# Optimization experiments

Measured on AMD Instinct MI355X. Metric: run time of the kernel, lower is better.

The kernel has to match this reference:

```python
import jax, jax.numpy as jnp
import numpy as np

B, S, H, HD, DM = 8, 1024, 16, 64, 1024

def rotate_half(x):
    x1, x2 = x[..., : x.shape[-1] // 2], x[..., x.shape[-1] // 2 :]
    return jnp.concatenate((-x2, x1), axis=-1)

def apply_rope(x, cos, sin):
    return x * cos + rotate_half(x) * sin

def setup_inputs() -> dict:
    key = jax.random.key(0)
    ks = jax.random.split(key, 6)
    T = B * S
    hidden_states = jax.random.normal(ks[0], (T, DM), dtype=jnp.float32)
    scale = 1.0 / np.sqrt(DM)
    q_w = jax.random.normal(ks[1], (DM, DM), dtype=jnp.float32) * scale
    k_w = jax.random.normal(ks[2], (DM, DM), dtype=jnp.float32) * scale
    v_w = jax.random.normal(ks[3], (DM, DM), dtype=jnp.float32) * scale
    o_w = jax.random.normal(ks[4], (DM, DM), dtype=jnp.float32) * scale
    # RoPE tables: positions restart at each segment boundary
    pos = jnp.tile(jnp.arange(S, dtype=jnp.float32), B)           # [T]
    inv_freq = 1.0 / (10000.0 ** (jnp.arange(0, HD, 2, dtype=jnp.float32) / HD))
    ang = pos[:, None] * inv_freq[None, :]                        # [T, HD/2]
    emb = jnp.concatenate([ang, ang], axis=-1)                    # [T, HD]
    cos = jnp.cos(emb)[:, None, :]                                # [T, 1, HD]
    sin = jnp.sin(emb)[:, None, :]
    cu_seqlens = (jnp.arange(B + 1) * S).astype(jnp.int32)        # [B+1]
    return {
        "hidden_states": hidden_states,
        "q_w": q_w, "k_w": k_w, "v_w": v_w, "o_w": o_w,
        "cos": cos, "sin": sin,
        "cu_seqlens": cu_seqlens, "max_seqlen": S,
    }

def reference(hidden_states, q_w, k_w, v_w, o_w, cos, sin, cu_seqlens, max_seqlen):
    T, D = hidden_states.shape
    hd = cos.shape[-1]
    nh = D // hd
    nb = cu_seqlens.shape[0] - 1
    S_ = max_seqlen
    # QKV projections (torch Linear: y = x @ W^T)
    q = (hidden_states @ q_w.T).reshape(T, nh, hd)
    k = (hidden_states @ k_w.T).reshape(T, nh, hd)
    v = (hidden_states @ v_w.T).reshape(T, nh, hd)
    q = apply_rope(q, cos, sin)
    k = apply_rope(k, cos, sin)
    # Equal-length varlen segments -> dense batched causal attention
    q = q.reshape(nb, S_, nh, hd)
    k = k.reshape(nb, S_, nh, hd)
    v = v.reshape(nb, S_, nh, hd)
    scale = 1.0 / np.sqrt(hd).astype(np.float32)
    scores = jnp.einsum("bqhd,bkhd->bhqk", q, k) * scale          # [B,H,S,S]
    causal = jnp.tril(jnp.ones((S_, S_), dtype=bool))
    scores = jnp.where(causal[None, None], scores, jnp.finfo(scores.dtype).min)
    probs = jax.nn.softmax(scores, axis=-1)
    attn = jnp.einsum("bhqk,bkhd->bqhd", probs, v).reshape(T, D)
    return attn @ o_w.T
```

## Files before the change

kernel.cpp:

```cpp
#include <hip/hip_runtime.h>

typedef __attribute__((ext_vector_type(8))) short short8;
typedef __attribute__((ext_vector_type(4))) short short4v;
typedef __attribute__((ext_vector_type(4))) float f32x4;

#define MFMA(a, b, c) __builtin_amdgcn_mfma_f32_16x16x32_bf16((a), (b), (c), 0, 0, 0)
#define GLD16(g, l)                                                            \
  __builtin_amdgcn_global_load_lds(                                            \
      (const __attribute__((address_space(1))) void*)(g),                      \
      (__attribute__((address_space(3))) void*)(l), 16, 0, 0)

static __device__ __forceinline__ float b2f(unsigned short b) {
  union { unsigned u; float f; } u; u.u = ((unsigned)b) << 16; return u.f;
}
static __device__ __forceinline__ unsigned short f2b(float f) {
  union { float f; unsigned u; } u; u.f = f;
  unsigned r = u.u + 0x7FFFu + ((u.u >> 16) & 1u);
  return (unsigned short)(r >> 16);
}
static __device__ __forceinline__ unsigned cvt_pk_bf16(float a, float b) {
  unsigned r;
  asm("v_cvt_pk_bf16_f32 %0, %1, %2" : "=v"(r) : "v"(a), "v"(b));
  return r;
}

__global__ __launch_bounds__(256) void convert_kernel(
    const float* __restrict__ hidden,
    const float* __restrict__ qw, const float* __restrict__ kw,
    const float* __restrict__ vw, const float* __restrict__ ow,
    unsigned short* __restrict__ dst) {
  const int HID4 = 2097152, W4 = 262144, TOT = HID4 + 4 * W4;
  for (int i = blockIdx.x * 256 + threadIdx.x; i < TOT; i += gridDim.x * 256) {
    const float* src; int off;
    if (i < HID4) { src = hidden; off = i; }
    else {
      int j = i - HID4; int w = j >> 18; off = j & (W4 - 1);
      src = (w == 0) ? qw : (w == 1) ? kw : (w == 2) ? vw : ow;
    }
    float4 v = *(const float4*)&src[(size_t)off * 4];
    short4v s;
    s[0] = (short)f2b(v.x); s[1] = (short)f2b(v.y);
    s[2] = (short)f2b(v.z); s[3] = (short)f2b(v.w);
    *(short4v*)&dst[(size_t)i * 4] = s;
  }
}

template <bool QKV>
__global__ __launch_bounds__(512, 2) void gemm256(
    const unsigned short* __restrict__ A,
    const unsigned short* __restrict__ W,
    void* __restrict__ Cv,
    const float* __restrict__ cosb, const float* __restrict__ sinb) {
  __shared__ __align__(16) unsigned short lds[73728];
  const int tid = threadIdx.x, wave = tid >> 6, lane = tid & 63;
  const int bm = blockIdx.x << 8, bnc = blockIdx.y << 7;
  const int wr = (wave >> 1) << 6, wc = (wave & 1) << 6;
  const int lr = lane & 15, hi4 = lane >> 4;
  const int rowb = tid >> 3;
  const int cgA = (tid & 7) ^ (rowb & 7);
  const unsigned short* aSrc = A + (size_t)(bm + rowb) * 1024 + (cgA << 3);
  const unsigned short* bSrc = W + (size_t)(bnc + rowb) * 1024 + (cgA << 3);

  f32x4 acc[4][4] = {};

#define STAGE(t, bi)                                                           \
  do {                                                                         \
    unsigned short* As_ = lds + (bi) * 24576;                                  \
    unsigned short* Bs_ = As_ + 16384;                                         \
    const int k0_ = (t) << 6;                                                  \
    _Pragma("unroll") for (int i = 0; i < 4; ++i)                              \
        GLD16(aSrc + (size_t)(i << 6) * 1024 + k0_,                            \
              As_ + (((i << 9) + tid) << 3));                                  \
    _Pragma("unroll") for (int j = 0; j < 2; ++j)                              \
        GLD16(bSrc + (size_t)(j << 6) * 1024 + k0_,                            \
              Bs_ + (((j << 9) + tid) << 3));                                  \
  } while (0)

  STAGE(0, 0);
  STAGE(1, 1);
  asm volatile("s_waitcnt vmcnt(6)" ::: "memory");
  __builtin_amdgcn_s_barrier();
  __builtin_amdgcn_sched_barrier(0);

  int bi = 0;
#pragma unroll
  for (int t = 0; t < 16; ++t) {
    int pf = bi + 2; if (pf >= 3) pf -= 3;
    const unsigned short* As = lds + bi * 24576;
    const unsigned short* Bs = As + 16384;
    unsigned short* Asp = lds + pf * 24576;
    unsigned short* Bsp = Asp + 16384;
    const int k2 = (t + 2) << 6;

    short8 afA[4], bfA[4];
#pragma unroll
    for (int x = 0; x < 4; ++x) {
      int ra = wr + x * 16 + lr;
      afA[x] = *(const short8*)&As[ra * 64 + ((hi4 ^ (ra & 7)) << 3)];
      int rb = wc + x * 16 + lr;
      bfA[x] = *(const short8*)&Bs[rb * 64 + ((hi4 ^ (rb & 7)) << 3)];
    }
    if (t < 14) {
#pragma unroll
      for (int i = 0; i < 2; ++i)
        GLD16(aSrc + (size_t)(i << 6) * 1024 + k2, Asp + (((i << 9) + tid) << 3));
      GLD16(bSrc + k2, Bsp + (tid << 3));
    }
    __builtin_amdgcn_sched_barrier(0);
    __builtin_amdgcn_s_barrier();
    asm volatile("s_waitcnt lgkmcnt(0)" ::: "memory");
    __builtin_amdgcn_sched_barrier(0);
    __builtin_amdgcn_s_setprio(1);
#pragma unroll
    for (int mm = 0; mm < 4; ++mm)
#pragma unroll
      for (int nn = 0; nn < 4; ++nn)
        acc[mm][nn] = MFMA(afA[mm], bfA[nn], acc[mm][nn]);
    __builtin_amdgcn_s_setprio(0);
    __builtin_amdgcn_sched_barrier(0);
    __builtin_amdgcn_s_barrier();

    short8 afB[4], bfB[4];
#pragma unroll
    for (int x = 0; x < 4; ++x) {
      int ra = wr + x * 16 + lr;
      afB[x] = *(const short8*)&As[ra * 64 + (((hi4 + 4) ^ (ra & 7)) << 3)];
      int rb = wc + x * 16 + lr;
      bfB[x] = *(const short8*)&Bs[rb * 64 + (((hi4 + 4) ^ (rb & 7)) << 3)];
    }
    if (t < 14) {
#pragma unroll
      for (int i = 2; i < 4; ++i)
        GLD16(aSrc + (size_t)(i << 6) * 1024 + k2, Asp + (((i << 9) + tid) << 3));
      GLD16(bSrc + (size_t)(1 << 6) * 1024 + k2, Bsp + (((1 << 9) + tid) << 3));
    }
    __builtin_amdgcn_sched_barrier(0);
    __builtin_amdgcn_s_barrier();
    asm volatile("s_waitcnt lgkmcnt(0)" ::: "memory");
    __builtin_amdgcn_sched_barrier(0);
    __builtin_amdgcn_s_setprio(1);
#pragma unroll
    for (int mm = 0; mm < 4; ++mm)
#pragma unroll
      for (int nn = 0; nn < 4; ++nn)
        acc[mm][nn] = MFMA(afB[mm], bfB[nn], acc[mm][nn]);
    __builtin_amdgcn_s_setprio(0);
    __builtin_amdgcn_sched_barrier(0);
    if (t < 14) asm volatile("s_waitcnt vmcnt(6)" ::: "memory");
    else        asm volatile("s_waitcnt vmcnt(0)" ::: "memory");
    __builtin_amdgcn_s_barrier();
    __builtin_amdgcn_sched_barrier(0);
    if (++bi == 3) bi = 0;
  }
#undef STAGE

  const int rg = hi4 << 2;
  if constexpr (QKV) {
    const int grp = bnc >> 10;
    unsigned short* Cbuf = (unsigned short*)Cv + (size_t)grp * 8388608;
    const int colbase = (bnc & 1023) + wc;
    if (grp < 2) {
      float* csf = (float*)lds;
      float* snf = csf + 8192;
#pragma unroll
      for (int i = 0; i < 4; ++i) {
        int s = (i << 9) + tid;
        int row = s >> 3, c4 = (s & 7) << 2;
        GLD16(cosb + (size_t)(bm + row) * 64 + c4, csf + s * 4);
        GLD16(sinb + (size_t)(bm + row) * 64 + c4, snf + s * 4);
      }
      asm volatile("s_waitcnt vmcnt(0)" ::: "memory");
      __builtin_amdgcn_s_barrier();
      __builtin_amdgcn_sched_barrier(0);
      const float sc = (grp == 0) ? 0.18033688011112042f : 1.0f;
#pragma unroll
      for (int mm = 0; mm < 4; ++mm)
#pragma unroll
        for (int r = 0; r < 4; ++r) {
          int rloc = wr + mm * 16 + rg + r;
          size_t rowoff = (size_t)(bm + rloc) * 1024;
#pragma unroll
          for (int nn = 0; nn < 2; ++nn) {
            int d = nn * 16 + lr;
            float c = csf[rloc * 32 + d], s2 = snf[rloc * 32 + d];
            float lo = acc[mm][nn][r], hi = acc[mm][nn + 2][r];
            Cbuf[rowoff + colbase + nn * 16 + lr]      = f2b((lo * c - hi * s2) * sc);
            Cbuf[rowoff + colbase + nn * 16 + lr + 32] = f2b((hi * c + lo * s2) * sc);
          }
        }
    } else {
#pragma unroll
      for (int mm = 0; mm < 4; ++mm)
#pragma unroll
        for (int nn = 0; nn < 4; ++nn)
#pragma unroll
          for (int r = 0; r < 4; ++r)
            Cbuf[(size_t)(bm + wr + mm * 16 + rg + r) * 1024 + colbase + nn * 16 + lr] =
                f2b(acc[mm][nn][r]);
    }
  } else {
    float* C = (float*)Cv;
#pragma unroll
    for (int mm = 0; mm < 4; ++mm)
#pragma unroll
      for (int nn = 0; nn < 4; ++nn)
#pragma unroll
        for (int r = 0; r < 4; ++r)
          C[(size_t)(bm + wr + mm * 16 + rg + r) * 1024 + bnc + wc + nn * 16 + lr] =
              acc[mm][nn][r];
  }
}

__global__ __launch_bounds__(256, 3) void attn_kernel(
    const unsigned short* __restrict__ Q,
    const unsigned short* __restrict__ K,
    const unsigned short* __restrict__ V,
    unsigned short* __restrict__ O) {
  __shared__ unsigned short Ks[2][64][72];
  __shared__ unsigned short Vt[2][64][72];
  const int tid = threadIdx.x, wave = tid >> 6, lane = tid & 63;
  const int idx = blockIdx.x;
  const int bh = idx & 127;
  const int b = bh >> 4, h = bh & 15;
  const int qb = 7 - (idx >> 7);
  const int tok0 = b << 10;
  const int lr = lane & 15, hi4 = lane >> 4, lk8 = hi4 << 3;
  const int rg = hi4 << 2;
  const int qrow0 = (qb << 7) + (wave << 5);

  short8 qf[2][2];
#pragma unroll
  for (int mt = 0; mt < 2; ++mt) {
    const unsigned short* qp = &Q[(size_t)(tok0 + qrow0 + mt * 16 + lr) * 1024 + h * 64];
#pragma unroll
    for (int kk = 0; kk < 2; ++kk) qf[mt][kk] = *(const short8*)&qp[kk * 32 + lk8];
  }

  f32x4 acc[2][4] = {};
  float m[2], l[2];
#pragma unroll
  for (int mt = 0; mt < 2; ++mt) { m[mt] = -1e30f; l[mt] = 0.f; }

  const int krow = tid >> 3, kcol = (tid & 7) << 3;
  const int vd = lane;
  const int baseC = ((wave & 1) << 4) + ((wave >> 1) << 2);
  short8 kst[2];
  short4v vst[4];

#define LOADT(kbx)                                                                 \
  do {                                                                             \
    const int kr0_ = tok0 + ((kbx) << 6);                                          \
    _Pragma("unroll") for (int it = 0; it < 2; ++it)                               \
        kst[it] = *(const short8*)&K[(size_t)(kr0_ + krow + it * 32) * 1024 +      \
                                     h * 64 + kcol];                               \
    _Pragma("unroll") for (int it = 0; it < 2; ++it) {                             \
      const unsigned short* vp_ =                                                  \
          &V[(size_t)(kr0_ + ((wave + it * 4) << 3)) * 1024 + h * 64 + vd];        \
      _Pragma("unroll") for (int i = 0; i < 4; ++i) {                              \
        vst[it * 2][i]     = (short)vp_[(size_t)i * 1024];                         \
        vst[it * 2 + 1][i] = (short)vp_[(size_t)(i + 4) * 1024];                   \
      }                                                                            \
    }                                                                              \
  } while (0)

#define STORET(bi)                                                                 \
  do {                                                                             \
    _Pragma("unroll") for (int it = 0; it < 2; ++it)                               \
        *(short8*)&Ks[bi][krow + it * 32][kcol] = kst[it];                         \
    *(short4v*)&Vt[bi][vd][baseC]          = vst[0];                               \
    *(short4v*)&Vt[bi][vd][baseC + 8]      = vst[1];                               \
    *(short4v*)&Vt[bi][vd][32 + baseC]     = vst[2];                               \
    *(short4v*)&Vt[bi][vd][32 + baseC + 8] = vst[3];                               \
  } while (0)

  const int nkb = (qb + 1) << 1;
  LOADT(0);
  STORET(0);
  __syncthreads();

  for (int kb = 0; kb < nkb; ++kb) {
    const int cur = kb & 1;
    const bool more = (kb + 1 < nkb);
    if (more) LOADT(kb + 1);

    float p[2][4][4];
#pragma unroll
    for (int ct = 0; ct < 4; ++ct) {
      short8 kf0 = *(const short8*)&Ks[cur][ct * 16 + lr][lk8];
      short8 kf1 = *(const short8*)&Ks[cur][ct * 16 + lr][32 + lk8];
      f32x4 s0 = {}, s1 = {};
      s0 = MFMA(kf0, qf[0][0], s0);
      s0 = MFMA(kf1, qf[0][1], s0);
      s1 = MFMA(kf0, qf[1][0], s1);
      s1 = MFMA(kf1, qf[1][1], s1);
#pragma unroll
      for (int r = 0; r < 4; ++r) { p[0][ct][r] = s0[r]; p[1][ct][r] = s1[r]; }
    }
    if (kb >= 2 * qb) {
#pragma unroll
      for (int mt = 0; mt < 2; ++mt) {
        const int qg = qrow0 + mt * 16 + lr;
#pragma unroll
        for (int ct = 0; ct < 4; ++ct)
#pragma unroll
          for (int r = 0; r < 4; ++r) {
            int kg = (kb << 6) + ct * 16 + rg + r;
            if (kg > qg) p[mt][ct][r] = -1e30f;
          }
      }
    }
    unsigned pk[2][4][2];
#pragma unroll
    for (int mt = 0; mt < 2; ++mt) {
      float lmx = p[mt][0][0];
#pragma unroll
      for (int ct = 0; ct < 4; ++ct)
#pragma unroll
        for (int r = 0; r < 4; ++r) lmx = fmaxf(lmx, p[mt][ct][r]);
      if (__any(lmx > m[mt] + 8.f)) {
        float mx = lmx;
        mx = fmaxf(mx, __shfl_xor(mx, 16));
        mx = fmaxf(mx, __shfl_xor(mx, 32));
        float mn = fmaxf(m[mt], mx);
        float alpha = __builtin_amdgcn_exp2f(m[mt] - mn);
        m[mt] = mn;
        l[mt] *= alpha;
        float a4[4];
#pragma unroll
        for (int r = 0; r < 4; ++r) a4[r] = __shfl(alpha, rg + r);
#pragma unroll
        for (int dt = 0; dt < 4; ++dt)
#pragma unroll
          for (int r = 0; r < 4; ++r) acc[mt][dt][r] *= a4[r];
      }
      float rs = 0.f;
#pragma unroll
      for (int ct = 0; ct < 4; ++ct) {
#pragma unroll
        for (int r = 0; r < 4; ++r) {
          p[mt][ct][r] = __builtin_amdgcn_exp2f(p[mt][ct][r] - m[mt]);
          rs += p[mt][ct][r];
        }
        pk[mt][ct][0] = cvt_pk_bf16(p[mt][ct][0], p[mt][ct][1]);
        pk[mt][ct][1] = cvt_pk_bf16(p[mt][ct][2], p[mt][ct][3]);
      }
      l[mt] += rs;
    }
#pragma unroll
    for (int kk = 0; kk < 2; ++kk) {
      union { unsigned u[4]; short8 v; } pa0, pa1;
      pa0.u[0] = pk[0][kk * 2][0];     pa0.u[1] = pk[0][kk * 2][1];
      pa0.u[2] = pk[0][kk * 2 + 1][0]; pa0.u[3] = pk[0][kk * 2 + 1][1];
      pa1.u[0] = pk[1][kk * 2][0];     pa1.u[1] = pk[1][kk * 2][1];
      pa1.u[2] = pk[1][kk * 2 + 1][0]; pa1.u[3] = pk[1][kk * 2 + 1][1];
#pragma unroll
      for (int dt = 0; dt < 4; ++dt) {
        short8 vf = *(const short8*)&Vt[cur][dt * 16 + lr][kk * 32 + lk8];
        acc[0][dt] = MFMA(pa0.v, vf, acc[0][dt]);
        acc[1][dt] = MFMA(pa1.v, vf, acc[1][dt]);
      }
    }

    if (more) {
      STORET(cur ^ 1);
      __syncthreads();
    }
  }
#undef LOADT
#undef STORET

#pragma unroll
  for (int mt = 0; mt < 2; ++mt) {
    float lsum = l[mt];
    lsum += __shfl_xor(lsum, 16);
    lsum += __shfl_xor(lsum, 32);
    float linv = 1.0f / lsum;
    float inv[4];
#pragma unroll
    for (int r = 0; r < 4; ++r) inv[r] = __shfl(linv, rg + r);
#pragma unroll
    for (int dt = 0; dt < 4; ++dt)
#pragma unroll
      for (int r = 0; r < 4; ++r) {
        int trow = tok0 + qrow0 + mt * 16 + rg + r;
        O[(size_t)trow * 1024 + h * 64 + dt * 16 + lr] = f2b(acc[mt][dt][r] * inv[r]);
      }
  }
}

extern "C" void kernel_launch(void* const* d_in, const int* in_sizes, int n_in,
                              void* d_out, int out_size, void* d_ws, size_t ws_size,
                              hipStream_t stream) {
  const float* hidden = (const float*)d_in[0];
  const float* q_w    = (const float*)d_in[1];
  const float* k_w    = (const float*)d_in[2];
  const float* v_w    = (const float*)d_in[3];
  const float* o_w    = (const float*)d_in[4];
  const float* cosb   = (const float*)d_in[5];
  const float* sinb   = (const float*)d_in[6];

  const size_t TD = (size_t)8192 * 1024;
  unsigned short* ws  = (unsigned short*)d_ws;
  unsigned short* Qb  = ws;
  unsigned short* Kb  = ws + TD;
  unsigned short* Vb  = ws + 2 * TD;
  unsigned short* hBF = ws + 3 * TD;
  unsigned short* wBF = ws + 4 * TD;

  convert_kernel<<<4096, 256, 0, stream>>>(hidden, q_w, k_w, v_w, o_w, hBF);
  gemm256<true><<<dim3(32, 24), 512, 0, stream>>>(hBF, wBF, Qb, cosb, sinb);
  attn_kernel<<<1024, 256, 0, stream>>>(Qb, Kb, Vb, hBF );
  gemm256<false><<<dim3(32, 8), 512, 0, stream>>>(
      hBF, wBF + 3 * 1048576, d_out, nullptr, nullptr);
}
```

Before: 127.1 us.

## Halve GEMM K-tile to 32 and raise occupancy to four blocks per CU

```diff
diff --git a/kernel.cpp b/kernel.cpp
--- a/kernel.cpp
+++ b/kernel.cpp
@@ -46,18 +46,18 @@
 }
 
 template <bool QKV>
-__global__ __launch_bounds__(512, 2) void gemm256(
+__global__ __launch_bounds__(512, 4) void gemm256(
     const unsigned short* __restrict__ A,
     const unsigned short* __restrict__ W,
     void* __restrict__ Cv,
     const float* __restrict__ cosb, const float* __restrict__ sinb) {
-  __shared__ __align__(16) unsigned short lds[73728];
+  __shared__ __align__(16) unsigned short lds[36864];
   const int tid = threadIdx.x, wave = tid >> 6, lane = tid & 63;
   const int bm = blockIdx.x << 8, bnc = blockIdx.y << 7;
   const int wr = (wave >> 1) << 6, wc = (wave & 1) << 6;
   const int lr = lane & 15, hi4 = lane >> 4;
-  const int rowb = tid >> 3;
-  const int cgA = (tid & 7) ^ (rowb & 7);
+  const int rowb = tid >> 2;
+  const int cgA = (tid & 3) ^ (rowb & 3);
   const unsigned short* aSrc = A + (size_t)(bm + rowb) * 1024 + (cgA << 3);
   const unsigned short* bSrc = W + (size_t)(bnc + rowb) * 1024 + (cgA << 3);
 
@@ -65,88 +65,45 @@
 
 #define STAGE(t, bi)                                                           \
   do {                                                                         \
-    unsigned short* As_ = lds + (bi) * 24576;                                  \
-    unsigned short* Bs_ = As_ + 16384;                                         \
-    const int k0_ = (t) << 6;                                                  \
-    _Pragma("unroll") for (int i = 0; i < 4; ++i)                              \
-        GLD16(aSrc + (size_t)(i << 6) * 1024 + k0_,                            \
+    unsigned short* As_ = lds + (bi) * 12288;                                  \
+    unsigned short* Bs_ = As_ + 8192;                                          \
+    const int k0_ = (t) << 5;                                                  \
+    _Pragma("unroll") for (int i = 0; i < 2; ++i)                              \
+        GLD16(aSrc + (size_t)(i << 7) * 1024 + k0_,                            \
               As_ + (((i << 9) + tid) << 3));                                  \
-    _Pragma("unroll") for (int j = 0; j < 2; ++j)                              \
-        GLD16(bSrc + (size_t)(j << 6) * 1024 + k0_,                            \
-              Bs_ + (((j << 9) + tid) << 3));                                  \
+    GLD16(bSrc + k0_, Bs_ + (tid << 3));                                       \
   } while (0)
 
   STAGE(0, 0);
   STAGE(1, 1);
-  asm volatile("s_waitcnt vmcnt(6)" ::: "memory");
+  asm volatile("s_waitcnt vmcnt(3)" ::: "memory");
   __builtin_amdgcn_s_barrier();
   __builtin_amdgcn_sched_barrier(0);
 
   int bi = 0;
 #pragma unroll
-  for (int t = 0; t < 16; ++t) {
+  for (int t = 0; t < 32; ++t) {
     int pf = bi + 2; if (pf >= 3) pf -= 3;
-    const unsigned short* As = lds + bi * 24576;
-    const unsigned short* Bs = As + 16384;
-    unsigned short* Asp = lds + pf * 24576;
-    unsigned short* Bsp = Asp + 16384;
-    const int k2 = (t + 2) << 6;
-
-    short8 afA[4], bfA[4];
+    if (t < 30) STAGE(t + 2, pf);
+    const unsigned short* As = lds + bi * 12288;
+    const unsigned short* Bs = As + 8192;
+    short8 af[4], bfr[4];
 #pragma unroll
     for (int x = 0; x < 4; ++x) {
       int ra = wr + x * 16 + lr;
-      afA[x] = *(const short8*)&As[ra * 64 + ((hi4 ^ (ra & 7)) << 3)];
+      af[x] = *(const short8*)&As[ra * 32 + ((hi4 ^ (ra & 3)) << 3)];
       int rb = wc + x * 16 + lr;
-      bfA[x] = *(const short8*)&Bs[rb * 64 + ((hi4 ^ (rb & 7)) << 3)];
-    }
-    if (t < 14) {
-#pragma unroll
-      for (int i = 0; i < 2; ++i)
-        GLD16(aSrc + (size_t)(i << 6) * 1024 + k2, Asp + (((i << 9) + tid) << 3));
-      GLD16(bSrc + k2, Bsp + (tid << 3));
-    }
-    __builtin_amdgcn_sched_barrier(0);
-    __builtin_amdgcn_s_barrier();
-    asm volatile("s_waitcnt lgkmcnt(0)" ::: "memory");
-    __builtin_amdgcn_sched_barrier(0);
+      bfr[x] = *(const short8*)&Bs[rb * 32 + ((hi4 ^ (rb & 3)) << 3)];
+    }
     __builtin_amdgcn_s_setprio(1);
 #pragma unroll
     for (int mm = 0; mm < 4; ++mm)
 #pragma unroll
       for (int nn = 0; nn < 4; ++nn)
-        acc[mm][nn] = MFMA(afA[mm], bfA[nn], acc[mm][nn]);
+        acc[mm][nn] = MFMA(af[mm], bfr[nn], acc[mm][nn]);
     __builtin_amdgcn_s_setprio(0);
     __builtin_amdgcn_sched_barrier(0);
-    __builtin_amdgcn_s_barrier();
-
-    short8 afB[4], bfB[4];
-#pragma unroll
-    for (int x = 0; x < 4; ++x) {
-      int ra = wr + x * 16 + lr;
-      afB[x] = *(const short8*)&As[ra * 64 + (((hi4 + 4) ^ (ra & 7)) << 3)];
-      int rb = wc + x * 16 + lr;
-      bfB[x] = *(const short8*)&Bs[rb * 64 + (((hi4 + 4) ^ (rb & 7)) << 3)];
-    }
-    if (t < 14) {
-#pragma unroll
-      for (int i = 2; i < 4; ++i)
-        GLD16(aSrc + (size_t)(i << 6) * 1024 + k2, Asp + (((i << 9) + tid) << 3));
-      GLD16(bSrc + (size_t)(1 << 6) * 1024 + k2, Bsp + (((1 << 9) + tid) << 3));
-    }
-    __builtin_amdgcn_sched_barrier(0);
-    __builtin_amdgcn_s_barrier();
-    asm volatile("s_waitcnt lgkmcnt(0)" ::: "memory");
-    __builtin_amdgcn_sched_barrier(0);
-    __builtin_amdgcn_s_setprio(1);
-#pragma unroll
-    for (int mm = 0; mm < 4; ++mm)
-#pragma unroll
-      for (int nn = 0; nn < 4; ++nn)
-        acc[mm][nn] = MFMA(afB[mm], bfB[nn], acc[mm][nn]);
-    __builtin_amdgcn_s_setprio(0);
-    __builtin_amdgcn_sched_barrier(0);
-    if (t < 14) asm volatile("s_waitcnt vmcnt(6)" ::: "memory");
+    if (t < 30) asm volatile("s_waitcnt vmcnt(3)" ::: "memory");
     else        asm volatile("s_waitcnt vmcnt(0)" ::: "memory");
     __builtin_amdgcn_s_barrier();
     __builtin_amdgcn_sched_barrier(0);
```

New measurement: 125.9 us. Within noise of the previous version (-1.0%).
